# Performance work log

Measured on AMD Instinct MI355X. Metric: run time of the kernel, lower is better.

The kernel has to match this reference:

```python
import jax, jax.numpy as jnp
import numpy as np

R2PI = float(np.sqrt(2.0 * np.pi))


def setup_inputs() -> dict:
    key = jax.random.key(0)
    k1, k2, k3 = jax.random.split(key, 3)
    B, T, D = 32, 512, 384
    feats = jax.random.normal(k1, (B, T, D), dtype=jnp.float32)
    # per-token Gaussian widths (positive, ~0.1..4.1 frames)
    rng = jax.random.uniform(k2, (B, T), dtype=jnp.float32) * 4.0 + 0.1
    # per-token durations in frames, 1..8
    durations = jax.random.randint(k3, (B, T), 1, 9, dtype=jnp.int32)
    # outlen = durations.sum(1).max() (torch uses .item(); static here)
    outlen = int(jnp.max(jnp.sum(durations, axis=1)))
    return {"feats": feats, "rng": rng, "durations": durations, "outlen": outlen}


def reference(feats, rng, durations, outlen):
    # feats: [B, T, D], rng: [B, T], durations: [B, T] int, outlen: python int
    d = durations.astype(feats.dtype)                     # [B, T]
    c = d / 2 + jnp.cumsum(d, axis=-1)                    # [B, T] gaussian centers
    r = rng + 1e-6                                        # [B, T]
    t = jnp.arange(outlen, dtype=feats.dtype)             # [outlen]
    # weights: [B, outlen, T]
    z = (t[None, :, None] - c[:, None, :]) / r[:, None, :]
    weights = jnp.exp(-0.5 * z * z) / (r[:, None, :] * R2PI) + 1e-6
    weights_normalized = weights / jnp.sum(weights, axis=2, keepdims=True)
    upsampled = jnp.matmul(weights_normalized, feats)     # [B, outlen, D]
    return upsampled
```

## Files before the change

kernel.cpp:

```cpp
#include <hip/hip_runtime.h>
#include <math.h>

#define BB 32
#define TT 512
#define DD 384
#define ROWS 48
#define NCOLS 192
#define WS 72
#define TSL 16
#define R2PI_INV 0.3989422804014327f
#define BAND 33.0f

typedef short bf16x8 __attribute__((ext_vector_type(8)));
typedef float f32x4  __attribute__((ext_vector_type(4)));

__device__ __forceinline__ ushort f2bf(float f) {
    unsigned u = __float_as_uint(f);
    u += 0x7fffu + ((u >> 16) & 1u);
    return (ushort)(u >> 16);
}

__global__ __launch_bounds__(384)
void prep_kernel(const float* __restrict__ feats,
                 const float* __restrict__ rng,
                 const int*   __restrict__ dur,
                 ushort* __restrict__ featsT,
                 float* __restrict__ cW,
                 float* __restrict__ irW,
                 float* __restrict__ colsumP)
{
    const int tid = threadIdx.x;
    const int tsl = blockIdx.x, b = blockIdx.y;

    if (tsl == 0 && tid >= 320) {
        const int ln = tid - 320;
        int4   da = ((const int4*)(dur + b * TT))[2 * ln];
        int4   db = ((const int4*)(dur + b * TT))[2 * ln + 1];
        float4 ra = ((const float4*)(rng + b * TT))[2 * ln];
        float4 rb = ((const float4*)(rng + b * TT))[2 * ln + 1];
        int   d8[8] = {da.x, da.y, da.z, da.w, db.x, db.y, db.z, db.w};
        float r8[8] = {ra.x, ra.y, ra.z, ra.w, rb.x, rb.y, rb.z, rb.w};
        int s8 = 0;
        #pragma unroll
        for (int j = 0; j < 8; ++j) s8 += d8[j];
        int p = s8;
        #pragma unroll
        for (int off = 1; off < 64; off <<= 1) {
            int n = __shfl_up(p, off);
            if (ln >= off) p += n;
        }
        int run = p - s8;
        float c8[8], i8[8];
        #pragma unroll
        for (int j = 0; j < 8; ++j) {
            run += d8[j];
            c8[j] = 0.5f * (float)d8[j] + (float)run;
            i8[j] = 1.0f / (r8[j] + 1e-6f);
        }
        float4* cO = (float4*)(cW + b * TT + 8 * ln);
        cO[0] = (float4){c8[0], c8[1], c8[2], c8[3]};
        cO[1] = (float4){c8[4], c8[5], c8[6], c8[7]};
        float4* iO = (float4*)(irW + b * TT + 8 * ln);
        iO[0] = (float4){i8[0], i8[1], i8[2], i8[3]};
        iO[1] = (float4){i8[4], i8[5], i8[6], i8[7]};
    }

    const int dd    = tid;
    const int tbase = tsl * 32;
    const float* fp = feats + ((size_t)b * TT + tbase) * DD + dd;
    float csum = 0.f;
    #pragma unroll
    for (int p = 0; p < 4; ++p) {
        float v[8];
        #pragma unroll
        for (int j = 0; j < 8; ++j) v[j] = fp[(size_t)(p * 8 + j) * DD];
        #pragma unroll
        for (int j = 0; j < 8; ++j) csum += v[j];
        uint4 pk;
        pk.x = (unsigned)f2bf(v[0]) | ((unsigned)f2bf(v[1]) << 16);
        pk.y = (unsigned)f2bf(v[2]) | ((unsigned)f2bf(v[3]) << 16);
        pk.z = (unsigned)f2bf(v[4]) | ((unsigned)f2bf(v[5]) << 16);
        pk.w = (unsigned)f2bf(v[6]) | ((unsigned)f2bf(v[7]) << 16);
        *(uint4*)(featsT + (((size_t)b * 64 + (tbase >> 3) + p) * DD + dd) * 8) = pk;
    }
    colsumP[((size_t)tsl * BB + b) * DD + dd] = csum;
}

__global__ __launch_bounds__(256)
void gemm_kernel(const ushort* __restrict__ featsT,
                 const float*  __restrict__ cW,
                 const float*  __restrict__ irW,
                 const float*  __restrict__ colsumP,
                 float* __restrict__ out, int O, int OB)
{
    __shared__ ushort sW[ROWS * WS];
    __shared__ float  sInv[ROWS];
    __shared__ float  sCS[NCOLS];

    const int tid = threadIdx.x;
    const int ln  = tid & 63, wv = tid >> 6;
    const int qd  = ln >> 4,  lm = ln & 15;

    const int id  = blockIdx.x;
    const int xcd = id & 7;
    const int s   = id >> 3;
    const int b   = (s / (OB * 2)) * 8 + xcd;
    const int r2  = s % (OB * 2);
    const int i0  = (r2 >> 1) * ROWS;
    const int nh  = r2 & 1;

    if (tid < NCOLS) {
        float t = 0.f;
        #pragma unroll
        for (int sl = 0; sl < TSL; ++sl)
            t += colsumP[((size_t)sl * BB + b) * DD + nh * NCOLS + tid];
        sCS[tid] = t * 1e-6f;
    }

    const float lo = (float)i0 - BAND;
    const float hi = (float)(i0 + ROWS - 1) + BAND;
    int cnt = 0;
    {
        const float4* cB = (const float4*)(cW + b * TT);
        float4 ca = cB[2 * ln], cb = cB[2 * ln + 1];
        float cv[8] = {ca.x, ca.y, ca.z, ca.w, cb.x, cb.y, cb.z, cb.w};
        #pragma unroll
        for (int j = 0; j < 8; ++j) {
            cnt += (cv[j] < lo) ? 1 : 0;
            cnt += (cv[j] <= hi) ? 0x10000 : 0;
        }
        #pragma unroll
        for (int off = 32; off >= 1; off >>= 1) cnt += __shfl_xor(cnt, off);
    }
    const int j_hi = cnt >> 16;
    const int j0   = (cnt & 0xffff) & ~7;
    int nc = (j_hi > j0) ? ((j_hi - j0 + 63) >> 6) : 0;
    if (nc < 1) nc = 1;

    f32x4 acc[3][3];
    #pragma unroll
    for (int r = 0; r < 3; ++r)
        #pragma unroll
        for (int nt = 0; nt < 3; ++nt)
            acc[r][nt] = (f32x4){0.f, 0.f, 0.f, 0.f};
    float rsum[12];
    #pragma unroll
    for (int rr = 0; rr < 12; ++rr) rsum[rr] = 0.f;

    const int colbase = nh * NCOLS + wv * 48 + lm;
    const ushort* bp = featsT + ((size_t)b * 64 * DD + colbase) * 8;
    const float tbase = (float)(i0 + wv * 12);

    for (int kc = 0; kc < nc; ++kc) {
        const int jt0 = j0 + (kc << 6);
        int kp0 = (jt0 >> 3) + qd;      if (kp0 > 63) kp0 = 63;
        int kp1 = (jt0 >> 3) + 4 + qd;  if (kp1 > 63) kp1 = 63;
        bf16x8 Bf[6];
        #pragma unroll
        for (int nt = 0; nt < 3; ++nt) Bf[nt]     = *(const bf16x8*)(bp + (size_t)kp0 * (DD * 8) + nt * 128);
        #pragma unroll
        for (int nt = 0; nt < 3; ++nt) Bf[3 + nt] = *(const bf16x8*)(bp + (size_t)kp1 * (DD * 8) + nt * 128);

        const int jt = jt0 + ln;
        const int jc = (jt < TT) ? jt : (TT - 1);
        const float c  = cW[b * TT + jc];
        const float ir = irW[b * TT + jc];
        const float sc0 = (jt < TT) ? (ir * R2PI_INV) : 0.0f;
        float z = (tbase - c) * ir;
        ushort h[12];
        #pragma unroll
        for (int rr = 0; rr < 12; ++rr) {
            float e = __expf(-0.5f * z * z) * sc0;
            rsum[rr] += e;
            h[rr] = f2bf(e);
            z += ir;
        }
        if (kc) __syncthreads();
        #pragma unroll
        for (int rr = 0; rr < 12; ++rr) sW[(wv * 12 + rr) * WS + ln] = h[rr];
        __syncthreads();

        #pragma unroll
        for (int ks = 0; ks < 2; ++ks)
            #pragma unroll
            for (int r = 0; r < 3; ++r) {
                bf16x8 A = *(const bf16x8*)&sW[(r * 16 + lm) * WS + ks * 32 + qd * 8];
                #pragma unroll
                for (int nt = 0; nt < 3; ++nt)
                    acc[r][nt] = __builtin_amdgcn_mfma_f32_16x16x32_bf16(A, Bf[ks * 3 + nt], acc[r][nt], 0, 0, 0);
            }
    }

    #pragma unroll
    for (int rr = 0; rr < 12; ++rr) {
        float t = rsum[rr];
        #pragma unroll
        for (int off = 32; off >= 1; off >>= 1) t += __shfl_xor(t, off);
        if (ln == 0) sInv[wv * 12 + rr] = 1.0f / (t + (float)TT * 1e-6f);
    }

    float csr[3];
    #pragma unroll
    for (int nt = 0; nt < 3; ++nt) csr[nt] = sCS[wv * 48 + lm + nt * 16];
    __syncthreads();

    #pragma unroll
    for (int r = 0; r < 3; ++r) {
        #pragma unroll
        for (int reg = 0; reg < 4; ++reg) {
            int lrow = r * 16 + qd * 4 + reg;
            int grow = i0 + lrow;
            if (grow < O) {
                float scl = sInv[lrow];
                float* op = out + ((size_t)b * O + grow) * DD + colbase;
                #pragma unroll
                for (int nt = 0; nt < 3; ++nt)
                    op[nt * 16] = (acc[r][nt][reg] + csr[nt]) * scl;
            }
        }
    }
}

extern "C" void kernel_launch(void* const* d_in, const int* in_sizes, int n_in,
                              void* d_out, int out_size, void* d_ws, size_t ws_size,
                              hipStream_t stream) {
    const float* feats = (const float*)d_in[0];
    const float* rng   = (const float*)d_in[1];
    const int*   dur   = (const int*)d_in[2];
    float* out = (float*)d_out;
    const int O = out_size / (BB * DD);
    const int OB = (O + ROWS - 1) / ROWS;

    ushort* featsT = (ushort*)d_ws;
    float*  cW  = (float*)((char*)d_ws + (size_t)BB * DD * TT * 2);
    float*  irW = cW + BB * TT;
    float*  colsumP = irW + BB * TT;

    dim3 pg(TSL, BB);
    prep_kernel<<<pg, 384, 0, stream>>>(feats, rng, dur, featsT, cW, irW, colsumP);
    gemm_kernel<<<OB * BB * 2, 256, 0, stream>>>(featsT, cW, irW, colsumP, out, O, OB);
}
```

Baseline: 161.7 us.

## Drop bf16 transposed feats buffer; convert fp32 feats on the fly in GEMM

The prep kernel no longer writes a packed bf16 transposed copy of feats. Instead the GEMM kernel loads fp32 feats directly (strided per-token scalar loads) and converts them to bf16 with v_cvt_pk_bf16_f32 before the MFMA. This removes a 12 MB write plus re-read of the intermediate buffer. In exchange the GEMM issues 48 scalar fp32 loads per lane per k-chunk instead of 6 vector loads, and reads twice the bytes for the band-limited region.

Result: slower. 173.9 us (+7.6%).

```diff
diff --git a/kernel.cpp b/kernel.cpp
--- a/kernel.cpp
+++ b/kernel.cpp
@@ -24,7 +24,6 @@
 void prep_kernel(const float* __restrict__ feats,
                  const float* __restrict__ rng,
                  const int*   __restrict__ dur,
-                 ushort* __restrict__ featsT,
                  float* __restrict__ cW,
                  float* __restrict__ irW,
                  float* __restrict__ colsumP)
@@ -76,18 +75,12 @@
         for (int j = 0; j < 8; ++j) v[j] = fp[(size_t)(p * 8 + j) * DD];
         #pragma unroll
         for (int j = 0; j < 8; ++j) csum += v[j];
-        uint4 pk;
-        pk.x = (unsigned)f2bf(v[0]) | ((unsigned)f2bf(v[1]) << 16);
-        pk.y = (unsigned)f2bf(v[2]) | ((unsigned)f2bf(v[3]) << 16);
-        pk.z = (unsigned)f2bf(v[4]) | ((unsigned)f2bf(v[5]) << 16);
-        pk.w = (unsigned)f2bf(v[6]) | ((unsigned)f2bf(v[7]) << 16);
-        *(uint4*)(featsT + (((size_t)b * 64 + (tbase >> 3) + p) * DD + dd) * 8) = pk;
     }
     colsumP[((size_t)tsl * BB + b) * DD + dd] = csum;
 }
 
 __global__ __launch_bounds__(256)
-void gemm_kernel(const ushort* __restrict__ featsT,
+void gemm_kernel(const float* __restrict__ feats,
                  const float*  __restrict__ cW,
                  const float*  __restrict__ irW,
                  const float*  __restrict__ colsumP,
@@ -148,18 +141,27 @@
     for (int rr = 0; rr < 12; ++rr) rsum[rr] = 0.f;
 
     const int colbase = nh * NCOLS + wv * 48 + lm;
-    const ushort* bp = featsT + ((size_t)b * 64 * DD + colbase) * 8;
+    const float* fbase = feats + (size_t)b * TT * DD + colbase;
     const float tbase = (float)(i0 + wv * 12);
 
     for (int kc = 0; kc < nc; ++kc) {
         const int jt0 = j0 + (kc << 6);
-        int kp0 = (jt0 >> 3) + qd;      if (kp0 > 63) kp0 = 63;
-        int kp1 = (jt0 >> 3) + 4 + qd;  if (kp1 > 63) kp1 = 63;
-        bf16x8 Bf[6];
-        #pragma unroll
-        for (int nt = 0; nt < 3; ++nt) Bf[nt]     = *(const bf16x8*)(bp + (size_t)kp0 * (DD * 8) + nt * 128);
-        #pragma unroll
-        for (int nt = 0; nt < 3; ++nt) Bf[3 + nt] = *(const bf16x8*)(bp + (size_t)kp1 * (DD * 8) + nt * 128);
+        const int t0k = jt0 + qd * 8;
+        float s0[3][8], s1[3][8];
+        #pragma unroll
+        for (int nt = 0; nt < 3; ++nt)
+            #pragma unroll
+            for (int j = 0; j < 8; ++j) {
+                int t = t0k + j;       if (t > TT - 1) t = TT - 1;
+                s0[nt][j] = fbase[(size_t)t * DD + nt * 16];
+            }
+        #pragma unroll
+        for (int nt = 0; nt < 3; ++nt)
+            #pragma unroll
+            for (int j = 0; j < 8; ++j) {
+                int t = t0k + 32 + j;  if (t > TT - 1) t = TT - 1;
+                s1[nt][j] = fbase[(size_t)t * DD + nt * 16];
+            }
 
         const int jt = jt0 + ln;
         const int jc = (jt < TT) ? jt : (TT - 1);
@@ -175,6 +177,20 @@
             h[rr] = f2bf(e);
             z += ir;
         }
+
+        bf16x8 Bf[6];
+        #pragma unroll
+        for (int nt = 0; nt < 3; ++nt) {
+            union { unsigned u[4]; bf16x8 v; } U0, U1;
+            #pragma unroll
+            for (int i = 0; i < 4; ++i) {
+                asm("v_cvt_pk_bf16_f32 %0, %1, %2" : "=v"(U0.u[i]) : "v"(s0[nt][2 * i]), "v"(s0[nt][2 * i + 1]));
+                asm("v_cvt_pk_bf16_f32 %0, %1, %2" : "=v"(U1.u[i]) : "v"(s1[nt][2 * i]), "v"(s1[nt][2 * i + 1]));
+            }
+            Bf[nt]     = U0.v;
+            Bf[3 + nt] = U1.v;
+        }
+
         if (kc) __syncthreads();
         #pragma unroll
         for (int rr = 0; rr < 12; ++rr) sW[(wv * 12 + rr) * WS + ln] = h[rr];
@@ -231,12 +247,11 @@
     const int O = out_size / (BB * DD);
     const int OB = (O + ROWS - 1) / ROWS;
 
-    ushort* featsT = (ushort*)d_ws;
-    float*  cW  = (float*)((char*)d_ws + (size_t)BB * DD * TT * 2);
-    float*  irW = cW + BB * TT;
-    float*  colsumP = irW + BB * TT;
+    float* cW  = (float*)d_ws;
+    float* irW = cW + BB * TT;
+    float* colsumP = irW + BB * TT;
 
     dim3 pg(TSL, BB);
-    prep_kernel<<<pg, 384, 0, stream>>>(feats, rng, dur, featsT, cW, irW, colsumP);
-    gemm_kernel<<<OB * BB * 2, 256, 0, stream>>>(featsT, cW, irW, colsumP, out, O, OB);
-}
+    prep_kernel<<<pg, 384, 0, stream>>>(feats, rng, dur, cW, irW, colsumP);
+    gemm_kernel<<<OB * BB * 2, 256, 0, stream>>>(feats, cW, irW, colsumP, out, O, OB);
+}
```
